# Optimization experiments

Hardware: AMD Instinct MI355X
Metric: run time of the kernel (lower is better)

Reference implementation:

```python
import jax, jax.numpy as jnp
import numpy as np

NUM_GRAPHS = 1024
NODES_PER_GRAPH = 9
EDGES_PER_GRAPH = NODES_PER_GRAPH * (NODES_PER_GRAPH - 1)  # 72, fully connected no self-loops
N = NUM_GRAPHS * NODES_PER_GRAPH
E = NUM_GRAPHS * EDGES_PER_GRAPH
POS_DIM = 64
HID = 256          # gnn_hidden_dim / common_gnn_dim
S1_FEAT = HID      # stage1 feature_dim (after projection)
S1_INT = S1_FEAT + POS_DIM           # 320
S2_FEAT = 2 * HID                    # 512 (two scales concatenated)
S2_OUT = 2 * HID                     # 512
S2_INT = S2_FEAT + POS_DIM           # 576
LN_EPS = 1e-5
SM_EPS = 1e-16  # PyG softmax eps


def _dense(x, w, b):
    return x @ w + b


def _layer_norm(x, g, b):
    mu = jnp.mean(x, axis=-1, keepdims=True)
    var = jnp.mean(jnp.square(x - mu), axis=-1, keepdims=True)
    return (x - mu) * jax.lax.rsqrt(var + LN_EPS) * g + b


def _segment_softmax(logits, idx, n):
    # logits: [E,1]; normalize over edges sharing the same destination node
    m = jax.ops.segment_max(logits, idx, num_segments=n)
    e = jnp.exp(logits - m[idx])
    s = jax.ops.segment_sum(e, idx, num_segments=n)
    return e / (s[idx] + SM_EPS)


def _gnn_layer(x, pos, src, dst, n, p):
    # x: [N, F], pos: [N, P]; edges src->dst (PyG: edge_index[0]=src j, edge_index[1]=dst i)
    ix = jnp.concatenate([x, pos], axis=-1)            # integrated_x [N, F+P]
    ii, ij = ix[dst], ix[src]                          # integrated_x_i / _j per edge
    # pairwise_fn(integrated_x_j, integrated_x_i) -> mlp(cat([integrated_x_i, integrated_x_j]))
    pw_in = jnp.concatenate([ii, ij], axis=-1)         # [E, 2*(F+P)]
    rel = _dense(jax.nn.gelu(_dense(pw_in, p['pw1_w'], p['pw1_b']), approximate=False),
                 p['pw2_w'], p['pw2_b'])               # [E, out]
    att_in = jnp.concatenate([x[dst], x[src], pos[dst], pos[src]], axis=-1)
    logits = _dense(jax.nn.leaky_relu(_dense(att_in, p['att1_w'], p['att1_b']), 0.01),
                    p['att2_w'], p['att2_b'])          # [E, 1]
    attw = _segment_softmax(logits, dst, n)
    aggr = jax.ops.segment_sum(attw * rel, dst, num_segments=n)  # [N, out]
    upd = jax.nn.gelu(_dense(jnp.concatenate([ix, aggr], axis=-1), p['upd_w'], p['upd_b']),
                      approximate=False)
    h = _dense(ix, p['skip_w'], p['skip_b']) + upd
    return _layer_norm(h, p['ln_g'], p['ln_b'])


def _glorot(key, shape):
    fan_in, fan_out = shape[0], shape[1]
    lim = np.sqrt(6.0 / (fan_in + fan_out))
    return jax.random.uniform(key, shape, jnp.float32, -lim, lim)


def setup_inputs() -> dict:
    key = jax.random.key(0)
    ks = iter(jax.random.split(key, 64))

    feat_low = jax.random.normal(next(ks), (N, 512), jnp.float32)
    feat_high = jax.random.normal(next(ks), (N, 1024), jnp.float32)
    batch_indices = jnp.repeat(jnp.arange(NUM_GRAPHS), NODES_PER_GRAPH).astype(jnp.int32)

    # fully connected (no self loop) edges within each 9-node graph
    loc = np.array([(j, i) for i in range(NODES_PER_GRAPH) for j in range(NODES_PER_GRAPH) if i != j],
                   dtype=np.int64)  # (src, dst)
    off = np.repeat(np.arange(NUM_GRAPHS) * NODES_PER_GRAPH, EDGES_PER_GRAPH)
    src = np.tile(loc[:, 0], NUM_GRAPHS) + off
    dst = np.tile(loc[:, 1], NUM_GRAPHS) + off
    edge_index = jnp.asarray(np.stack([src, dst]), dtype=jnp.int32)  # [2, E]

    inp = dict(feat_low=feat_low, feat_high=feat_high,
               batch_indices=batch_indices, edge_index=edge_index)

    inp['pos_table'] = jax.random.normal(next(ks), (NODES_PER_GRAPH, POS_DIM), jnp.float32)
    inp['proj_low_w'] = _glorot(next(ks), (512, HID)); inp['proj_low_b'] = jnp.zeros((HID,), jnp.float32)
    inp['proj_high_w'] = _glorot(next(ks), (1024, HID)); inp['proj_high_b'] = jnp.zeros((HID,), jnp.float32)

    def layer_params(pref, fdim, pdim, out):
        integ = fdim + pdim
        d = {}
        d[pref + 'pw1_w'] = _glorot(next(ks), (2 * integ, out)); d[pref + 'pw1_b'] = jnp.zeros((out,), jnp.float32)
        d[pref + 'pw2_w'] = _glorot(next(ks), (out, out)); d[pref + 'pw2_b'] = jnp.zeros((out,), jnp.float32)
        d[pref + 'att1_w'] = _glorot(next(ks), (2 * fdim + 2 * pdim, out)); d[pref + 'att1_b'] = jnp.zeros((out,), jnp.float32)
        d[pref + 'att2_w'] = _glorot(next(ks), (out, 1)); d[pref + 'att2_b'] = jnp.zeros((1,), jnp.float32)
        d[pref + 'upd_w'] = _glorot(next(ks), (integ + out, out)); d[pref + 'upd_b'] = jnp.zeros((out,), jnp.float32)
        d[pref + 'ln_g'] = jnp.ones((out,), jnp.float32); d[pref + 'ln_b'] = jnp.zeros((out,), jnp.float32)
        d[pref + 'skip_w'] = _glorot(next(ks), (integ, out)); d[pref + 'skip_b'] = jnp.zeros((out,), jnp.float32)
        return d

    inp.update(layer_params('s1_', S1_FEAT, POS_DIM, HID))
    inp.update(layer_params('s2_', S2_FEAT, POS_DIM, S2_OUT))

    inp['cls1_w'] = _glorot(next(ks), (S2_OUT, HID)); inp['cls1_b'] = jnp.zeros((HID,), jnp.float32)
    inp['cls2_w'] = _glorot(next(ks), (HID, 1)); inp['cls2_b'] = jnp.zeros((1,), jnp.float32)
    return inp


def _forward(feat_low, feat_high, pos_table,
             proj_low_w, proj_low_b, proj_high_w, proj_high_b,
             s1, s2, cls1_w, cls1_b, cls2_w, cls2_b,
             batch_indices, edge_index):
    src, dst = edge_index[0], edge_index[1]
    pos_ids = jnp.tile(jnp.arange(NODES_PER_GRAPH), NUM_GRAPHS)
    pos = pos_table[pos_ids]                                  # [N, P]
    h_low = _gnn_layer(_dense(feat_low, proj_low_w, proj_low_b), pos, src, dst, N, s1)
    h_high = _gnn_layer(_dense(feat_high, proj_high_w, proj_high_b), pos, src, dst, N, s1)
    unified = jnp.concatenate([h_low, h_high], axis=-1)       # [N, 512]
    h2 = _gnn_layer(unified, pos, src, dst, N, s2)            # [N, 512]
    pooled = jax.ops.segment_sum(h2, batch_indices, num_segments=NUM_GRAPHS)
    hid = jax.nn.gelu(_dense(pooled, cls1_w, cls1_b), approximate=False)
    return _dense(hid, cls2_w, cls2_b)                        # [G, 1]


S1_KEYS = ['pw1_w', 'pw1_b', 'pw2_w', 'pw2_b', 'att1_w', 'att1_b', 'att2_w', 'att2_b',
           'upd_w', 'upd_b', 'ln_g', 'ln_b', 'skip_w', 'skip_b']


def reference(feat_low, feat_high, batch_indices, edge_index, pos_table,
              proj_low_w, proj_low_b, proj_high_w, proj_high_b,
              s1_pw1_w, s1_pw1_b, s1_pw2_w, s1_pw2_b, s1_att1_w, s1_att1_b,
              s1_att2_w, s1_att2_b, s1_upd_w, s1_upd_b, s1_ln_g, s1_ln_b,
              s1_skip_w, s1_skip_b,
              s2_pw1_w, s2_pw1_b, s2_pw2_w, s2_pw2_b, s2_att1_w, s2_att1_b,
              s2_att2_w, s2_att2_b, s2_upd_w, s2_upd_b, s2_ln_g, s2_ln_b,
              s2_skip_w, s2_skip_b,
              cls1_w, cls1_b, cls2_w, cls2_b):
    s1 = dict(zip(S1_KEYS, [s1_pw1_w, s1_pw1_b, s1_pw2_w, s1_pw2_b, s1_att1_w, s1_att1_b,
                            s1_att2_w, s1_att2_b, s1_upd_w, s1_upd_b, s1_ln_g, s1_ln_b,
                            s1_skip_w, s1_skip_b]))
    s2 = dict(zip(S1_KEYS, [s2_pw1_w, s2_pw1_b, s2_pw2_w, s2_pw2_b, s2_att1_w, s2_att1_b,
                            s2_att2_w, s2_att2_b, s2_upd_w, s2_upd_b, s2_ln_g, s2_ln_b,
                            s2_skip_w, s2_skip_b]))
    return _forward(feat_low, feat_high, pos_table,
                    proj_low_w, proj_low_b, proj_high_w, proj_high_b,
                    s1, s2, cls1_w, cls1_b, cls2_w, cls2_b,
                    batch_indices, edge_index)
```

## Files before the change

### kernel.cpp

```cpp
#include <hip/hip_runtime.h>
#include <math.h>

#define NUM_GRAPHS 1024
#define NPG 9
#define NN 9216
#define NN2 18432
#define POSD 64

typedef __attribute__((ext_vector_type(8))) short bf16x8;
typedef __attribute__((ext_vector_type(4))) float f32x4;

__device__ __forceinline__ float gelu_f(float x) {
    return 0.5f * x * (1.0f + erff(x * 0.70710678118654752f));
}
__device__ __forceinline__ float gelu_fast(float x) {
    float y2 = 1.5957691216f * x * (1.0f + 0.044715f * x * x);
    float t = __expf(fminf(y2, 80.f));
    return x * t * __frcp_rn(t + 1.0f);
}
__device__ __forceinline__ ushort f2b(float v) {
    unsigned u = __float_as_uint(v);
    return (ushort)((u + 0x7fffu + ((u >> 16) & 1u)) >> 16);
}
__device__ __forceinline__ float b2f(ushort u) {
    return __uint_as_float(((unsigned)u) << 16);
}
__device__ __forceinline__ void gload16(const ushort* g, ushort* l) {
    __builtin_amdgcn_global_load_lds((const __attribute__((address_space(1))) void*)g,
                                     (__attribute__((address_space(3))) void*)l, 16, 0, 0);
}

__global__ __launch_bounds__(256, 3) void mgemm(
    const ushort* __restrict__ A, int lda,
    const ushort* __restrict__ Wt, int ldw,
    const float* __restrict__ bias1,
    const float* __restrict__ prow, int ldp,
    ushort* __restrict__ outB, int ldo, int K)
{
    __shared__ ushort smem[24576];
    const int wv = threadIdx.x >> 6, lane = threadIdx.x & 63;
    const int rh = wv & 1, ch = wv >> 1;

    const int GX = gridDim.x;
    const int nwg = GX * gridDim.y;
    const int flat = blockIdx.y * GX + blockIdx.x;
    const int swq = nwg >> 3, swr = nwg & 7;
    const int xcd = flat & 7, posi = flat >> 3;
    const int tix = (xcd < swr ? xcd * (swq + 1) : swr * (swq + 1) + (xcd - swr) * swq) + posi;
    const int m0 = (tix / GX) * 128, n0 = (tix % GX) * 128;

    f32x4 acc[4][4];
#pragma unroll
    for (int i = 0; i < 4; i++)
#pragma unroll
        for (int j = 0; j < 4; j++) acc[i][j] = (f32x4){0.f, 0.f, 0.f, 0.f};

    const ushort* Ab = A + (size_t)m0 * lda;
    const ushort* Wb = Wt + (size_t)n0 * ldw;

    auto stage = [&](int b, int k0) {
        ushort* sA = smem + b * 4096;
        ushort* sB = smem + 12288 + b * 4096;
#pragma unroll
        for (int i = 0; i < 2; i++) {
            int c = wv * 2 + i;
            int u = c * 64 + lane;
            int row = u >> 2, p = u & 3;
            int q = (p - (row >> 1)) & 3;
            gload16(Ab + (size_t)row * lda + k0 + q * 8, sA + c * 512);
            gload16(Wb + (size_t)row * ldw + k0 + q * 8, sB + c * 512);
        }
    };

    const int nsteps = K >> 5;
    stage(0, 0);
    stage(1, 32);
    int cur = 0;
    for (int s = 0; s < nsteps; s++) {
        if (s + 1 < nsteps) {
            asm volatile("s_waitcnt vmcnt(4)" ::: "memory");
        } else {
            asm volatile("s_waitcnt vmcnt(0)" ::: "memory");
        }
        __builtin_amdgcn_s_barrier();
        __builtin_amdgcn_sched_barrier(0);
        if (s + 2 < nsteps) {
            int nb = cur + 2; if (nb >= 3) nb -= 3;
            stage(nb, (s + 2) << 5);
        }

        const ushort* sA = smem + cur * 4096;
        const ushort* sB = smem + 12288 + cur * 4096;
        const int qg = lane >> 4;
        bf16x8 af[4], bfr[4];
#pragma unroll
        for (int bi = 0; bi < 4; bi++) {
            int r = rh * 64 + bi * 16 + (lane & 15);
            af[bi] = *(const bf16x8*)(sA + (r * 4 + ((qg + (r >> 1)) & 3)) * 8);
        }
#pragma unroll
        for (int bj = 0; bj < 4; bj++) {
            int r = ch * 64 + bj * 16 + (lane & 15);
            bfr[bj] = *(const bf16x8*)(sB + (r * 4 + ((qg + (r >> 1)) & 3)) * 8);
        }
        __builtin_amdgcn_s_setprio(1);
#pragma unroll
        for (int bi = 0; bi < 4; bi++)
#pragma unroll
            for (int bj = 0; bj < 4; bj++)
                acc[bi][bj] = __builtin_amdgcn_mfma_f32_16x16x32_bf16(
                    af[bi], bfr[bj], acc[bi][bj], 0, 0, 0);
        __builtin_amdgcn_s_setprio(0);
        __builtin_amdgcn_sched_barrier(0);
        cur++; if (cur >= 3) cur -= 3;
    }

    __syncthreads();
    float* sP = (float*)smem;
    const bool haveP = (prow != 0);
    if (haveP) {
        for (int i = threadIdx.x; i < 9 * 128; i += 256) {
            int rr = i >> 7, c = i & 127;
            sP[rr * 129 + c] = prow[(size_t)rr * ldp + n0 + c] + bias1[n0 + c];
        }
        __syncthreads();
    }
    ushort* T = smem + 4096;
#pragma unroll
    for (int bi = 0; bi < 4; bi++) {
#pragma unroll
        for (int r = 0; r < 4; r++) {
            int row = rh * 64 + bi * 16 + (lane >> 4) * 4 + r;
            int r9 = (m0 + row) % 9;
#pragma unroll
            for (int bj = 0; bj < 4; bj++) {
                int col = ch * 64 + bj * 16 + (lane & 15);
                float v = acc[bi][bj][r];
                if (haveP) v += sP[r9 * 129 + col];
                T[row * 136 + col] = f2b(v);
            }
        }
    }
    __syncthreads();
    {
        int row = threadIdx.x >> 1, half = threadIdx.x & 1;
        const ushort* src = T + row * 136 + half * 64;
        ushort* dst = outB + (size_t)(m0 + row) * ldo + n0 + half * 64;
#pragma unroll
        for (int j = 0; j < 8; j++)
            *(bf16x8*)(dst + j * 8) = *(const bf16x8*)(src + j * 8);
    }
}

struct PJArg {
    const ushort* A[2];
    const ushort* W[2];
    const float*  bias[2];
    ushort*       out[2];
    int lda[2], K[2];
};

__global__ __launch_bounds__(256, 3) void pjgemm(PJArg pa)
{
    __shared__ ushort sA[3][128 * 32];
    __shared__ ushort sB[3][128 * 32];
    const int z = blockIdx.z;
    const ushort* __restrict__ A  = pa.A[z];
    const ushort* __restrict__ Wt = pa.W[z];
    const float*  __restrict__ bias = pa.bias[z];
    ushort* out = pa.out[z];
    const int lda = pa.lda[z], ldw = lda, K = pa.K[z];

    const int wv = threadIdx.x >> 6, lane = threadIdx.x & 63;
    const int rh = wv & 1, ch = wv >> 1;

    const int GX = gridDim.x;
    const int nwg = GX * gridDim.y;
    const int flat = blockIdx.y * GX + blockIdx.x;
    const int swq = nwg >> 3, swr = nwg & 7;
    const int xcd = flat & 7, posi = flat >> 3;
    const int tix = (xcd < swr ? xcd * (swq + 1) : swr * (swq + 1) + (xcd - swr) * swq) + posi;
    const int m0 = (tix / GX) * 128, n0 = (tix % GX) * 128;

    f32x4 acc[4][4];
#pragma unroll
    for (int i = 0; i < 4; i++)
#pragma unroll
        for (int j = 0; j < 4; j++) acc[i][j] = (f32x4){0.f, 0.f, 0.f, 0.f};

    const ushort* Ab = A + (size_t)m0 * lda;
    const ushort* Wb = Wt + (size_t)n0 * ldw;

    auto stage = [&](int b, int k0) {
#pragma unroll
        for (int i = 0; i < 2; i++) {
            int c = wv * 2 + i;
            int u = c * 64 + lane;
            int row = u >> 2, p = u & 3;
            int q = (p - (row >> 1)) & 3;
            gload16(Ab + (size_t)row * lda + k0 + q * 8, sA[b] + c * 512);
            gload16(Wb + (size_t)row * ldw + k0 + q * 8, sB[b] + c * 512);
        }
    };
// ... 45 lines not shown
    __syncthreads();

#pragma unroll
    for (int bi = 0; bi < 4; bi++) {
#pragma unroll
        for (int r = 0; r < 4; r++) {
            int m = m0 + rh * 64 + bi * 16 + (lane >> 4) * 4 + r;
#pragma unroll
            for (int bj = 0; bj < 4; bj++) {
                int nc = ch * 64 + bj * 16 + (lane & 15);
                float v = acc[bi][bj][r] + sBias[nc];
                out[(size_t)m * 512 + n0 + nc] = f2b(v);
            }
        }
    }
}

#define NJOBS 16
struct TJobsArg {
    const float* src[NJOBS];
    long dst[NJOBS];
    int K[NJOBS], N[NJOBS], off0[NJOBS], ldo[NJOBS];
};

__global__ __launch_bounds__(256) void tw_kernel(TJobsArg ja, ushort* wbuf)
{
    int j = blockIdx.y;
    int K = ja.K[j], N = ja.N[j];
    int tk = K >> 5, tn = N >> 5;
    int t = blockIdx.x;
    if (t >= tk * tn) return;
    int kt = t % tk, nt = t / tk;
    const float* src = ja.src[j];
    ushort* out = wbuf + ja.dst[j];
    int ldo = ja.ldo[j];
    __shared__ float L[32][33];
    int r = threadIdx.x >> 5, c = threadIdx.x & 31;
#pragma unroll
    for (int rr = 0; rr < 4; rr++) {
        int k = kt * 32 + rr * 8 + r;
        L[rr * 8 + r][c] = src[(size_t)(ja.off0[j] + k) * N + nt * 32 + c];
    }
    __syncthreads();
#pragma unroll
    for (int rr = 0; rr < 4; rr++) {
        int n = nt * 32 + rr * 8 + r;
        out[(size_t)n * ldo + kt * 32 + c] = f2b(L[c][rr * 8 + r]);
    }
}

template<int O>
__global__ __launch_bounds__(256) void edge_kernel_t(
    const ushort* __restrict__ PB, const float* __restrict__ att2_w,
    ushort* __restrict__ Gout, int ldG, float* __restrict__ S)
{
    constexpr int O2 = O * 2, O5 = O * 5;
    constexpr int tpr = O >> 8;
    constexpr int tcount = 9 * tpr;
    constexpr int nch = O >> 3;
    constexpr int cshift = (O == 256) ? 5 : 6;
    constexpr int E = O >> 6;
    __shared__ ushort sPB[9 * O2];
    __shared__ float sAw[O];
    __shared__ float logits[72];
    __shared__ float aw[72];
    const int g = blockIdx.x;
    const int tid = threadIdx.x, lane = tid & 63, wave = tid >> 6;
    const ushort* gbase = PB + (size_t)g * 9 * O5;

    for (int i = wave; i < tcount; i += 4) {
        int row = i / tpr, co = i - row * tpr;
        gload16(gbase + (size_t)row * O5 + O2 + co * 512 + lane * 8, sPB + i * 512);
    }
    for (int c = tid; c < O; c += 256) sAw[c] = att2_w[c];
    __syncthreads();

    for (int e = wave; e < 72; e += 4) {
        int d = e >> 3, k = e & 7;
        int s = k + (k >= d);
        const ushort* ad = sPB + d * O2 + lane * E;
        const ushort* as = sPB + s * O2 + O + lane * E;
        const float* wp = sAw + lane * E;
        float p = 0.f;
        if constexpr (E == 4) {
            ushort4 a4 = *(const ushort4*)ad;
            ushort4 s4 = *(const ushort4*)as;
            float4 w4 = *(const float4*)wp;
            const ushort* ap = (const ushort*)&a4;
            const ushort* sp = (const ushort*)&s4;
            const float* wf = (const float*)&w4;
#pragma unroll
            for (int j = 0; j < 4; j++) {
                float v = b2f(ap[j]) + b2f(sp[j]);
                v = fmaxf(v, 0.01f * v);
                p += v * wf[j];
            }
        } else {
            bf16x8 a8 = *(const bf16x8*)ad;
            bf16x8 s8 = *(const bf16x8*)as;
            float4 w0 = *(const float4*)wp;
            float4 w1 = *(const float4*)(wp + 4);
            const ushort* ap = (const ushort*)&a8;
            const ushort* sp = (const ushort*)&s8;
            const float wf[8] = {w0.x, w0.y, w0.z, w0.w, w1.x, w1.y, w1.z, w1.w};
#pragma unroll
            for (int j = 0; j < 8; j++) {
                float v = b2f(ap[j]) + b2f(sp[j]);
                v = fmaxf(v, 0.01f * v);
                p += v * wf[j];
            }
        }
#pragma unroll
        for (int off = 32; off; off >>= 1) p += __shfl_down(p, off, 64);
        if (lane == 0) logits[e] = p;
    }
    __syncthreads();

    for (int i = wave; i < tcount; i += 4) {
        int row = i / tpr, co = i - row * tpr;
        gload16(gbase + (size_t)row * O5 + co * 512 + lane * 8, sPB + i * 512);
    }

    if (tid < 9) {
        float m = -INFINITY;
#pragma unroll
        for (int k = 0; k < 8; k++) m = fmaxf(m, logits[tid * 8 + k]);
        float s = 0.f, ee[8];
#pragma unroll
        for (int k = 0; k < 8; k++) { ee[k] = expf(logits[tid * 8 + k] - m); s += ee[k]; }
        float inv = 1.0f / (s + 1e-16f);
#pragma unroll
        for (int k = 0; k < 8; k++) aw[tid * 8 + k] = ee[k] * inv;
        S[g * 9 + tid] = s * inv;
    }
    __syncthreads();

    for (int idx = tid; idx < 9 * nch; idx += 256) {
        int n = idx >> cshift, cc = idx & (nch - 1);
        bf16x8 pdv = *(const bf16x8*)(sPB + n * O2 + cc * 8);
        const ushort* pp = (const ushort*)&pdv;
        float pdf[8];
#pragma unroll
        for (int j = 0; j < 8; j++) pdf[j] = b2f(pp[j]);
        float acc8[8];
#pragma unroll
        for (int j = 0; j < 8; j++) acc8[j] = 0.f;
#pragma unroll
        for (int k = 0; k < 8; k++) {
            int s = k + (k >= n);
            float w = aw[n * 8 + k];
            bf16x8 psv = *(const bf16x8*)(sPB + s * O2 + O + cc * 8);
            const ushort* qp = (const ushort*)&psv;
#pragma unroll
            for (int j = 0; j < 8; j++)
                acc8[j] += w * gelu_fast(pdf[j] + b2f(qp[j]));
        }
        ushort o8[8];
#pragma unroll
        for (int j = 0; j < 8; j++) o8[j] = f2b(acc8[j]);
        *(bf16x8*)(Gout + (size_t)(g * 9 + n) * ldG + cc * 8) = *(const bf16x8*)o8;
    }
}

__global__ __launch_bounds__(256) void ln_kernel(
    const ushort* __restrict__ P0,
    const float* __restrict__ ub, const float* __restrict__ vb,
    const float* __restrict__ S, const float* __restrict__ posU,
    const ushort* __restrict__ PBs, int ld5,
    const float* __restrict__ gw, const float* __restrict__ bw,
    ushort* outB, int ldoB, int rowsplit, float* outF, int O)
{
    const int wid = threadIdx.x >> 6, lane = threadIdx.x & 63;
    const int n = blockIdx.x * 4 + wid;
    const float sv = S[n];
    const ushort* p0 = P0 + (size_t)n * O;
    const ushort* sr = PBs + (size_t)n * ld5;
    const float* pu = posU + (size_t)(n % 9) * O;
    const int q = O >> 6;
    const int c0 = lane * q;

    float vals[8];
    float sum = 0.f;
    if (O == 256) {
        ushort4 pv = *(const ushort4*)(p0 + c0);
        ushort4 sk = *(const ushort4*)(sr + c0);
        float4 uu = *(const float4*)(ub + c0);
        float4 vv = *(const float4*)(vb + c0);
        float4 gg = *(const float4*)(pu + c0);
        const ushort tp[4] = {pv.x, pv.y, pv.z, pv.w};
        const ushort ts[4] = {sk.x, sk.y, sk.z, sk.w};
        const float tu[4] = {uu.x, uu.y, uu.z, uu.w};
        const float tv[4] = {vv.x, vv.y, vv.z, vv.w};
        const float tg[4] = {gg.x, gg.y, gg.z, gg.w};
#pragma unroll
        for (int j = 0; j < 4; j++) {
            float t = b2f(tp[j]) + tu[j] + tv[j] * sv + tg[j];
            vals[j] = gelu_f(t) + b2f(ts[j]);
            sum += vals[j];
        }
    } else {
        bf16x8 pv = *(const bf16x8*)(p0 + c0);
        bf16x8 sk = *(const bf16x8*)(sr + c0);
        const ushort* tp = (const ushort*)&pv;
        const ushort* ts = (const ushort*)&sk;
        float4 u0 = *(const float4*)(ub + c0), u1 = *(const float4*)(ub + c0 + 4);
        float4 v0 = *(const float4*)(vb + c0), v1 = *(const float4*)(vb + c0 + 4);
        float4 g0 = *(const float4*)(pu + c0), g1 = *(const float4*)(pu + c0 + 4);
        const float tu[8] = {u0.x,u0.y,u0.z,u0.w, u1.x,u1.y,u1.z,u1.w};
        const float tv[8] = {v0.x,v0.y,v0.z,v0.w, v1.x,v1.y,v1.z,v1.w};
        const float tg[8] = {g0.x,g0.y,g0.z,g0.w, g1.x,g1.y,g1.z,g1.w};
#pragma unroll
        for (int j = 0; j < 8; j++) {
            float t = b2f(tp[j]) + tu[j] + tv[j] * sv + tg[j];
            vals[j] = gelu_f(t) + b2f(ts[j]);
            sum += vals[j];
        }
    }

#pragma unroll
    for (int off = 32; off; off >>= 1) sum += __shfl_xor(sum, off, 64);
    const float mu = sum / (float)O;
    float var = 0.f;
#pragma unroll
    for (int j = 0; j < 8; j++) {
        if (j < q) { float d = vals[j] - mu; var += d * d; }
    }
#pragma unroll
    for (int off = 32; off; off >>= 1) var += __shfl_xor(var, off, 64);
    const float rstd = rsqrtf(var / (float)O + 1e-5f);

    int orow = n, coloff = 0;
    if (n >= rowsplit) { orow = n - rowsplit; coloff = 256; }

    if (outB) {
        ushort o[8];
#pragma unroll
        for (int j = 0; j < 8; j++) {
            if (j < q) o[j] = f2b((vals[j] - mu) * rstd * gw[c0 + j] + bw[c0 + j]);
        }
        ushort* dst = outB + (size_t)orow * ldoB + coloff + c0;
        if (q == 4) *(ushort4*)dst = *(const ushort4*)o;
        else        *(bf16x8*)dst = *(const bf16x8*)o;
    }
    if (outF) {
        float* dst = outF + (size_t)n * O + c0;
#pragma unroll
        for (int j = 0; j < 8; j++) {
            if (j < q) dst[j] = (vals[j] - mu) * rstd * gw[c0 + j] + bw[c0 + j];
        }
    }
}

__global__ void prep_kernel(
    const float* __restrict__ pw1_b1, const float* __restrict__ att1_b1, const float* __restrict__ skip_b1,
    const float* __restrict__ pw1_b2, const float* __restrict__ att1_b2, const float* __restrict__ skip_b2,
    const float* __restrict__ pos_table,
    const float* __restrict__ s1_pw1, const float* __restrict__ s1_att, const float* __restrict__ s1_skp,
    const float* __restrict__ s2_pw1, const float* __restrict__ s2_att, const float* __restrict__ s2_skp,
    const float* __restrict__ pw2_b1, const float* __restrict__ upd_w1,
    const float* __restrict__ pw2_b2, const float* __restrict__ upd_w2,
    const float* __restrict__ pw2_w1, const float* __restrict__ pw2_w2,
    const float* __restrict__ feat_low, const float* __restrict__ feat_high,
    float* biasC1, float* biasC2,
    float* posPB1, float* posPB2, float* posU1, float* posU2,
    float* vb1, float* vb2, ushort* pw2f1, ushort* pw2f2, ushort* featB)
{
// ... 97 lines not shown
        ushort4 o;
        o.x = f2b(v.x); o.y = f2b(v.y); o.z = f2b(v.z); o.w = f2b(v.w);
        ((ushort4*)(featB + (size_t)NN * 512))[i] = o;
    }
}

__global__ __launch_bounds__(256) void head_kernel(
    const float* __restrict__ h2,
    const float* __restrict__ cls1_w, const float* __restrict__ cls1_b,
    const float* __restrict__ cls2_w, const float* __restrict__ cls2_b,
    float* __restrict__ out)
{
    __shared__ float pooled[4][512];
    __shared__ float hid[4][256];
    const int b = blockIdx.x, tid = threadIdx.x;

    for (int idx = tid; idx < 4 * 512; idx += 256) {
        int gi = idx >> 9, c = idx & 511;
        const float* base = h2 + (size_t)((b * 4 + gi) * 9) * 512 + c;
        float s = 0.f;
#pragma unroll
        for (int k = 0; k < NPG; k++) s += base[(size_t)k * 512];
        pooled[gi][c] = s;
    }
    __syncthreads();

    {
        float acc[4] = {0.f, 0.f, 0.f, 0.f};
        for (int c = 0; c < 512; c++) {
            float w = cls1_w[(size_t)c * 256 + tid];
#pragma unroll
            for (int gi = 0; gi < 4; gi++) acc[gi] += pooled[gi][c] * w;
        }
        float bb = cls1_b[tid];
#pragma unroll
        for (int gi = 0; gi < 4; gi++) hid[gi][tid] = gelu_f(acc[gi] + bb);
    }
    __syncthreads();

    {
        int gi = tid >> 6, lane = tid & 63;
        float p = 0.f;
#pragma unroll
        for (int i = 0; i < 4; i++) p += hid[gi][lane + 64 * i] * cls2_w[lane + 64 * i];
#pragma unroll
        for (int off = 32; off; off >>= 1) p += __shfl_down(p, off, 64);
        if (lane == 0) out[b * 4 + gi] = p + cls2_b[0];
    }
}

static inline void mg(hipStream_t st, int M, int N, int K,
                      const ushort* A, int lda, const ushort* Wt, int ldw,
                      const float* bias1, const float* prow, int ldp,
                      ushort* outB, int ldo)
{
    dim3 grid(N / 128, M / 128);
    mgemm<<<grid, dim3(256), 0, st>>>(A, lda, Wt, ldw, bias1, prow, ldp,
                                      outB, ldo, K);
}

extern "C" void kernel_launch(void* const* d_in, const int* in_sizes, int n_in,
                              void* d_out, int out_size, void* d_ws, size_t ws_size,
                              hipStream_t stream)
{
    (void)in_sizes; (void)n_in; (void)out_size; (void)ws_size;
    const float* feat_low   = (const float*)d_in[0];
    const float* feat_high  = (const float*)d_in[1];
    const float* pos_table  = (const float*)d_in[4];
    const float* proj_low_w  = (const float*)d_in[5];
    const float* proj_low_b  = (const float*)d_in[6];
    const float* proj_high_w = (const float*)d_in[7];
    const float* proj_high_b = (const float*)d_in[8];
    const float* cls1_w = (const float*)d_in[37];
    const float* cls1_b = (const float*)d_in[38];
    const float* cls2_w = (const float*)d_in[39];
    const float* cls2_b = (const float*)d_in[40];
    float* out = (float*)d_out;

    const float* s1_pw1 = (const float*)d_in[9];
    const float* s1_att = (const float*)d_in[13];
    const float* s1_upd = (const float*)d_in[17];
    const float* s1_skp = (const float*)d_in[21];
    const float* s2_pw1 = (const float*)d_in[23];
    const float* s2_att = (const float*)d_in[27];
    const float* s2_upd = (const float*)d_in[31];
    const float* s2_skp = (const float*)d_in[35];

    const float* att2_w1 = (const float*)d_in[15];
    const float* upd_b1  = (const float*)d_in[18];
    const float* ln_g1   = (const float*)d_in[19];
    const float* ln_b1   = (const float*)d_in[20];
    const float* att2_w2 = (const float*)d_in[29];
    const float* upd_b2  = (const float*)d_in[32];
    const float* ln_g2   = (const float*)d_in[33];
    const float* ln_b2   = (const float*)d_in[34];

    char* base = (char*)d_ws;
    size_t cur = 0;
    auto alloc = [&](size_t bytes) { void* p = base + cur; cur += (bytes + 255) & ~(size_t)255; return p; };
    void*   PBreg = alloc((size_t)NN * 2560 * 2);
    ushort* PB    = (ushort*)PBreg;
    ushort* featB = (ushort*)PBreg;
    void*   IX1reg = alloc((size_t)NN2 * 512 * 2);
    ushort* ixa1  = (ushort*)IX1reg;
    float*  h2    = (float*)IX1reg;
    ushort* ixa2  = (ushort*)alloc((size_t)NN * 1024 * 2);
    ushort* PT    = (ushort*)alloc((size_t)NN2 * 512 * 2);
    float*  S     = (float*)alloc((size_t)NN2 * 4);
    float*  biasC1 = (float*)alloc(1280 * 4);
    float*  biasC2 = (float*)alloc(2560 * 4);
    float*  posPB1 = (float*)alloc(9 * 1280 * 4);
    float*  posPB2 = (float*)alloc(9 * 2560 * 4);
    float*  posU1  = (float*)alloc(9 * 256 * 4);
    float*  posU2  = (float*)alloc(9 * 512 * 4);
    float*  vb1   = (float*)alloc(256 * 4);
    float*  vb2   = (float*)alloc(512 * 4);
    ushort* wbuf  = (ushort*)alloc((size_t)3400000 * 2);

    TJobsArg ja;
    long woff[16];
    {
        struct J { const float* s; int K, N, off0, ldo; long sz; };
        J js[NJOBS] = {
            {proj_low_w,  512, 256, 0, 512, 512L * 256},
            {proj_high_w, 1024, 256, 0, 1024, 1024L * 256},
            {s1_pw1, 256, 256, 0, 256, 256L * 256},
            {s1_pw1, 256, 256, 320, 256, 256L * 256},
            {s1_att, 256, 256, 0, 256, 256L * 256},
            {s1_att, 256, 256, 256, 256, 256L * 256},
            {s1_skp, 256, 256, 0, 256, 256L * 256},
            {s1_upd, 256, 256, 0, 512, 512L * 256},
            {s1_upd, 256, 256, 320, 256, 256L * 256},
            {s2_pw1, 512, 512, 0, 512, 512L * 512},
            {s2_pw1, 512, 512, 576, 512, 512L * 512},
            {s2_att, 512, 512, 0, 512, 512L * 512},
            {s2_att, 512, 512, 512, 512, 512L * 512},
            {s2_skp, 512, 512, 0, 512, 512L * 512},
            {s2_upd, 512, 512, 0, 1024, 1024L * 512},
            {s2_upd, 512, 512, 576, 512, 512L * 512},
        };
        long off = 0;
        for (int i = 0; i < NJOBS; i++) {
            ja.src[i] = js[i].s; ja.K[i] = js[i].K; ja.N[i] = js[i].N;
            ja.off0[i] = js[i].off0; ja.ldo[i] = js[i].ldo;
            ja.dst[i] = off; woff[i] = off;
            off += js[i].sz;
        }
    }
    long pw2off1 = woff[15] + 512L * 512;
    long pw2off2 = pw2off1 + 256L * 256;
    tw_kernel<<<dim3(256, NJOBS), dim3(256), 0, stream>>>(ja, wbuf);

    ushort* wBig5_1 = wbuf + woff[2];
    ushort* updW1   = wbuf + woff[7];
    ushort* updbT1  = wbuf + woff[8];
    ushort* wBig5_2 = wbuf + woff[9];
    ushort* updW2   = wbuf + woff[14];
    ushort* updbT2  = wbuf + woff[15];
    ushort* pw2f1   = wbuf + pw2off1;
    ushort* pw2f2   = wbuf + pw2off2;

    {
        long tot = 1280 + 2560 + 9 * 1280 + 9 * 2560 + 9 * 256 + 9 * 512
                 + 256 + 512 + 256 * 256 + 512 * 512
                 + (long)NN * 512 / 4 + (long)NN * 1024 / 4;
        prep_kernel<<<dim3((unsigned)((tot + 255) / 256)), dim3(256), 0, stream>>>(
            (const float*)d_in[10], (const float*)d_in[14], (const float*)d_in[22],
            (const float*)d_in[24], (const float*)d_in[28], (const float*)d_in[36],
            pos_table,
            s1_pw1, s1_att, s1_skp, s2_pw1, s2_att, s2_skp,
            (const float*)d_in[12], s1_upd, (const float*)d_in[26], s2_upd,
            (const float*)d_in[11], (const float*)d_in[25],
            feat_low, feat_high,
            biasC1, biasC2, posPB1, posPB2, posU1, posU2, vb1, vb2, pw2f1, pw2f2, featB);
    }

    mg(stream, 256, 256, 256, updbT1, 256, pw2f1, 256, 0, 0, 0, updW1 + 256, 512);
    mg(stream, 512, 512, 512, updbT2, 512, pw2f2, 512, 0, 0, 0, updW2 + 512, 1024);

    {
        PJArg pa;
        pa.A[0] = featB;                      pa.lda[0] = 512;  pa.K[0] = 512;
        pa.A[1] = featB + (size_t)NN * 512;   pa.lda[1] = 1024; pa.K[1] = 1024;
        pa.W[0] = wbuf + woff[0];
        pa.W[1] = wbuf + woff[1];
        pa.bias[0] = proj_low_b;
        pa.bias[1] = proj_high_b;
        pa.out[0] = ixa1;
        pa.out[1] = ixa1 + (size_t)NN * 512;
        pjgemm<<<dim3(2, NN / 128, 2), dim3(256), 0, stream>>>(pa);
    }

    mg(stream, NN2, 1280, 256, ixa1, 512, wBig5_1, 256, biasC1, posPB1, 1280, PB, 1280);
    edge_kernel_t<256><<<dim3(2 * NUM_GRAPHS), dim3(256), 0, stream>>>(
        PB, att2_w1, ixa1 + 256, 512, S);
    mg(stream, NN2, 256, 512, ixa1, 512, updW1, 512, 0, 0, 0, PT, 256);
    ln_kernel<<<dim3(NN2 / 4), dim3(256), 0, stream>>>(
        PT, upd_b1, vb1, S, posU1,
        PB + 4 * 256, 1280, ln_g1, ln_b1, ixa2, 1024, NN, 0, 256);

    mg(stream, NN, 2560, 512, ixa2, 1024, wBig5_2, 512, biasC2, posPB2, 2560, PB, 2560);
    edge_kernel_t<512><<<dim3(NUM_GRAPHS), dim3(256), 0, stream>>>(
        PB, att2_w2, ixa2 + 512, 1024, S);
    mg(stream, NN, 512, 1024, ixa2, 1024, updW2, 1024, 0, 0, 0, PT, 512);
    ln_kernel<<<dim3(NN / 4), dim3(256), 0, stream>>>(
        PT, upd_b2, vb2, S, posU2,
        PB + 4 * 512, 2560, ln_g2, ln_b2, 0, 0, 1 << 30, h2, 512);

    head_kernel<<<dim3(NUM_GRAPHS / 4), dim3(256), 0, stream>>>(h2, cls1_w, cls1_b, cls2_w, cls2_b, out);
}
```

Baseline: 522.6 us.

## Enlarge mgemm tile to 256x128 with 8 waves and double buffering

The general GEMM kernel now uses 512 threads (8 waves) per block, each block covering 256 rows by 128 columns, so each staged weight tile is reused across twice as many rows. The three-stage LDS pipeline becomes a two-buffer scheme that waits on all outstanding loads every step. The epilogue writes the output in two 128-row passes through shared memory. This cuts weight reloads and halves the number of blocks, at the cost of less latency hiding in the K loop and fewer blocks, which can leave CUs idle when M is small.

```diff
diff --git a/kernel.cpp b/kernel.cpp
--- a/kernel.cpp
+++ b/kernel.cpp
@@ -30,7 +30,7 @@
                                      (__attribute__((address_space(3))) void*)l, 16, 0, 0);
 }
 
-__global__ __launch_bounds__(256, 3) void mgemm(
+__global__ __launch_bounds__(512, 4) void mgemm(
     const ushort* __restrict__ A, int lda,
     const ushort* __restrict__ Wt, int ldw,
     const float* __restrict__ bias1,
@@ -39,7 +39,7 @@
 {
     __shared__ ushort smem[24576];
     const int wv = threadIdx.x >> 6, lane = threadIdx.x & 63;
-    const int rh = wv & 1, ch = wv >> 1;
+    const int wr = wv >> 1, wc = wv & 1;
 
     const int GX = gridDim.x;
     const int nwg = GX * gridDim.y;
@@ -47,7 +47,7 @@
     const int swq = nwg >> 3, swr = nwg & 7;
     const int xcd = flat & 7, posi = flat >> 3;
     const int tix = (xcd < swr ? xcd * (swq + 1) : swr * (swq + 1) + (xcd - swr) * swq) + posi;
-    const int m0 = (tix / GX) * 128, n0 = (tix % GX) * 128;
+    const int m0 = (tix / GX) * 256, n0 = (tix % GX) * 128;
 
     f32x4 acc[4][4];
 #pragma unroll
@@ -59,8 +59,8 @@
     const ushort* Wb = Wt + (size_t)n0 * ldw;
 
     auto stage = [&](int b, int k0) {
-        ushort* sA = smem + b * 4096;
-        ushort* sB = smem + 12288 + b * 4096;
+        ushort* sA = smem + b * 8192;
+        ushort* sB = smem + 16384 + b * 4096;
 #pragma unroll
         for (int i = 0; i < 2; i++) {
             int c = wv * 2 + i;
@@ -68,39 +68,36 @@
             int row = u >> 2, p = u & 3;
             int q = (p - (row >> 1)) & 3;
             gload16(Ab + (size_t)row * lda + k0 + q * 8, sA + c * 512);
+        }
+        {
+            int c = wv;
+            int u = c * 64 + lane;
+            int row = u >> 2, p = u & 3;
+            int q = (p - (row >> 1)) & 3;
             gload16(Wb + (size_t)row * ldw + k0 + q * 8, sB + c * 512);
         }
     };
 
     const int nsteps = K >> 5;
     stage(0, 0);
-    stage(1, 32);
-    int cur = 0;
     for (int s = 0; s < nsteps; s++) {
-        if (s + 1 < nsteps) {
-            asm volatile("s_waitcnt vmcnt(4)" ::: "memory");
-        } else {
-            asm volatile("s_waitcnt vmcnt(0)" ::: "memory");
-        }
+        asm volatile("s_waitcnt vmcnt(0)" ::: "memory");
         __builtin_amdgcn_s_barrier();
         __builtin_amdgcn_sched_barrier(0);
-        if (s + 2 < nsteps) {
-            int nb = cur + 2; if (nb >= 3) nb -= 3;
-            stage(nb, (s + 2) << 5);
-        }
-
-        const ushort* sA = smem + cur * 4096;
-        const ushort* sB = smem + 12288 + cur * 4096;
+        if (s + 1 < nsteps) stage((s + 1) & 1, (s + 1) << 5);
+
+        const ushort* sA = smem + (s & 1) * 8192;
+        const ushort* sB = smem + 16384 + (s & 1) * 4096;
         const int qg = lane >> 4;
         bf16x8 af[4], bfr[4];
 #pragma unroll
         for (int bi = 0; bi < 4; bi++) {
-            int r = rh * 64 + bi * 16 + (lane & 15);
+            int r = wr * 64 + bi * 16 + (lane & 15);
             af[bi] = *(const bf16x8*)(sA + (r * 4 + ((qg + (r >> 1)) & 3)) * 8);
         }
 #pragma unroll
         for (int bj = 0; bj < 4; bj++) {
-            int r = ch * 64 + bj * 16 + (lane & 15);
+            int r = wc * 64 + bj * 16 + (lane & 15);
             bfr[bj] = *(const bf16x8*)(sB + (r * 4 + ((qg + (r >> 1)) & 3)) * 8);
         }
         __builtin_amdgcn_s_setprio(1);
@@ -112,43 +109,50 @@
                     af[bi], bfr[bj], acc[bi][bj], 0, 0, 0);
         __builtin_amdgcn_s_setprio(0);
         __builtin_amdgcn_sched_barrier(0);
-        cur++; if (cur >= 3) cur -= 3;
     }
 
     __syncthreads();
     float* sP = (float*)smem;
     const bool haveP = (prow != 0);
     if (haveP) {
-        for (int i = threadIdx.x; i < 9 * 128; i += 256) {
+        for (int i = threadIdx.x; i < 9 * 128; i += 512) {
             int rr = i >> 7, c = i & 127;
             sP[rr * 129 + c] = prow[(size_t)rr * ldp + n0 + c] + bias1[n0 + c];
         }
         __syncthreads();
     }
-    ushort* T = smem + 4096;
-#pragma unroll
-    for (int bi = 0; bi < 4; bi++) {
-#pragma unroll
-        for (int r = 0; r < 4; r++) {
-            int row = rh * 64 + bi * 16 + (lane >> 4) * 4 + r;
-            int r9 = (m0 + row) % 9;
-#pragma unroll
-            for (int bj = 0; bj < 4; bj++) {
-                int col = ch * 64 + bj * 16 + (lane & 15);
-                float v = acc[bi][bj][r];
-                if (haveP) v += sP[r9 * 129 + col];
-                T[row * 136 + col] = f2b(v);
+    ushort* T = smem + 2560;
+#pragma unroll
+    for (int pass = 0; pass < 2; pass++) {
+        if ((wv >> 2) == pass) {
+            int rbase = (wr & 1) * 64;
+#pragma unroll
+            for (int bi = 0; bi < 4; bi++) {
+#pragma unroll
+                for (int r = 0; r < 4; r++) {
+                    int row_l = rbase + bi * 16 + (lane >> 4) * 4 + r;
+                    int r9 = (m0 + pass * 128 + row_l) % 9;
+#pragma unroll
+                    for (int bj = 0; bj < 4; bj++) {
+                        int col = wc * 64 + bj * 16 + (lane & 15);
+                        float v = acc[bi][bj][r];
+                        if (haveP) v += sP[r9 * 129 + col];
+                        T[row_l * 136 + col] = f2b(v);
+                    }
+                }
             }
         }
-    }
-    __syncthreads();
-    {
-        int row = threadIdx.x >> 1, half = threadIdx.x & 1;
-        const ushort* src = T + row * 136 + half * 64;
-        ushort* dst = outB + (size_t)(m0 + row) * ldo + n0 + half * 64;
-#pragma unroll
-        for (int j = 0; j < 8; j++)
-            *(bf16x8*)(dst + j * 8) = *(const bf16x8*)(src + j * 8);
+        __syncthreads();
+        {
+            int row_l = threadIdx.x >> 2, qq = threadIdx.x & 3;
+            const ushort* src = T + row_l * 136 + qq * 32;
+            ushort* dst = outB + (size_t)(m0 + pass * 128 + row_l) * ldo + n0 + qq * 32;
+            *(bf16x8*)(dst) = *(const bf16x8*)(src);
+            *(bf16x8*)(dst + 8) = *(const bf16x8*)(src + 8);
+            *(bf16x8*)(dst + 16) = *(const bf16x8*)(src + 16);
+            *(bf16x8*)(dst + 24) = *(const bf16x8*)(src + 24);
+        }
+        if (pass == 0) __syncthreads();
     }
 }
 
@@ -665,8 +669,8 @@
                       const float* bias1, const float* prow, int ldp,
                       ushort* outB, int ldo)
 {
-    dim3 grid(N / 128, M / 128);
-    mgemm<<<grid, dim3(256), 0, st>>>(A, lda, Wt, ldw, bias1, prow, ldp,
+    dim3 grid(N / 128, M / 256);
+    mgemm<<<grid, dim3(512), 0, st>>>(A, lda, Wt, ldw, bias1, prow, ldp,
                                       outB, ldo, K);
 }
 
```

Result: slower. 537.6 us (+2.9%).

## Make mgemm waves independent 64x64 tiles with per-wave double-buffered LDS

Applied to the files above, without the earlier changes.

The GEMM kernel moves from one 128x128 tile per block, with four waves sharing a triple-buffered LDS pipeline, to each wave owning its own 64x64 output tile with a private double-buffered LDS region. This removes all block-level barriers in the main loop and the epilogue, and the launch becomes a flattened 1D grid with XCD swizzle over wave tiles. The cost is that operand tiles are no longer shared across waves, so global and LDS traffic per FLOP roughly doubles. Occupancy hints also drop from 3 to 2 blocks per CU.

```diff
diff --git a/kernel.cpp b/kernel.cpp
--- a/kernel.cpp
+++ b/kernel.cpp
@@ -30,24 +30,25 @@
                                      (__attribute__((address_space(3))) void*)l, 16, 0, 0);
 }
 
-__global__ __launch_bounds__(256, 3) void mgemm(
+__global__ __launch_bounds__(256, 2) void mgemm(
     const ushort* __restrict__ A, int lda,
     const ushort* __restrict__ Wt, int ldw,
     const float* __restrict__ bias1,
     const float* __restrict__ prow, int ldp,
-    ushort* __restrict__ outB, int ldo, int K)
+    ushort* __restrict__ outB, int ldo, int K, int NT)
 {
-    __shared__ ushort smem[24576];
+    __shared__ ushort smem[4][8192];
     const int wv = threadIdx.x >> 6, lane = threadIdx.x & 63;
-    const int rh = wv & 1, ch = wv >> 1;
-
-    const int GX = gridDim.x;
-    const int nwg = GX * gridDim.y;
-    const int flat = blockIdx.y * GX + blockIdx.x;
+    ushort* wb = smem[wv];
+
+    const int nwg = gridDim.x;
+    const int flat = blockIdx.x;
     const int swq = nwg >> 3, swr = nwg & 7;
     const int xcd = flat & 7, posi = flat >> 3;
-    const int tix = (xcd < swr ? xcd * (swq + 1) : swr * (swq + 1) + (xcd - swr) * swq) + posi;
-    const int m0 = (tix / GX) * 128, n0 = (tix % GX) * 128;
+    const int btix = (xcd < swr ? xcd * (swq + 1) : swr * (swq + 1) + (xcd - swr) * swq) + posi;
+    const int w = btix * 4 + wv;
+    const int mt = w / NT, nt = w - mt * NT;
+    const int m0 = mt * 64, n0 = nt * 64;
 
     f32x4 acc[4][4];
 #pragma unroll
@@ -59,48 +60,41 @@
     const ushort* Wb = Wt + (size_t)n0 * ldw;
 
     auto stage = [&](int b, int k0) {
-        ushort* sA = smem + b * 4096;
-        ushort* sB = smem + 12288 + b * 4096;
-#pragma unroll
-        for (int i = 0; i < 2; i++) {
-            int c = wv * 2 + i;
-            int u = c * 64 + lane;
-            int row = u >> 2, p = u & 3;
+#pragma unroll
+        for (int c = 0; c < 4; c++) {
+            int row = c * 16 + (lane >> 2), p = lane & 3;
             int q = (p - (row >> 1)) & 3;
-            gload16(Ab + (size_t)row * lda + k0 + q * 8, sA + c * 512);
-            gload16(Wb + (size_t)row * ldw + k0 + q * 8, sB + c * 512);
+            gload16(Ab + (size_t)row * lda + k0 + q * 8, wb + b * 2048 + c * 512);
+        }
+#pragma unroll
+        for (int c = 0; c < 4; c++) {
+            int row = c * 16 + (lane >> 2), p = lane & 3;
+            int q = (p - (row >> 1)) & 3;
+            gload16(Wb + (size_t)row * ldw + k0 + q * 8, wb + 4096 + b * 2048 + c * 512);
         }
     };
 
     const int nsteps = K >> 5;
     stage(0, 0);
-    stage(1, 32);
-    int cur = 0;
     for (int s = 0; s < nsteps; s++) {
         if (s + 1 < nsteps) {
-            asm volatile("s_waitcnt vmcnt(4)" ::: "memory");
+            stage((s + 1) & 1, (s + 1) << 5);
+            asm volatile("s_waitcnt vmcnt(8)" ::: "memory");
         } else {
             asm volatile("s_waitcnt vmcnt(0)" ::: "memory");
         }
-        __builtin_amdgcn_s_barrier();
-        __builtin_amdgcn_sched_barrier(0);
-        if (s + 2 < nsteps) {
-            int nb = cur + 2; if (nb >= 3) nb -= 3;
-            stage(nb, (s + 2) << 5);
-        }
-
-        const ushort* sA = smem + cur * 4096;
-        const ushort* sB = smem + 12288 + cur * 4096;
+        const ushort* sA = wb + (s & 1) * 2048;
+        const ushort* sB = wb + 4096 + (s & 1) * 2048;
         const int qg = lane >> 4;
         bf16x8 af[4], bfr[4];
 #pragma unroll
         for (int bi = 0; bi < 4; bi++) {
-            int r = rh * 64 + bi * 16 + (lane & 15);
+            int r = bi * 16 + (lane & 15);
             af[bi] = *(const bf16x8*)(sA + (r * 4 + ((qg + (r >> 1)) & 3)) * 8);
         }
 #pragma unroll
         for (int bj = 0; bj < 4; bj++) {
-            int r = ch * 64 + bj * 16 + (lane & 15);
+            int r = bj * 16 + (lane & 15);
             bfr[bj] = *(const bf16x8*)(sB + (r * 4 + ((qg + (r >> 1)) & 3)) * 8);
         }
         __builtin_amdgcn_s_setprio(1);
@@ -111,44 +105,38 @@
                 acc[bi][bj] = __builtin_amdgcn_mfma_f32_16x16x32_bf16(
                     af[bi], bfr[bj], acc[bi][bj], 0, 0, 0);
         __builtin_amdgcn_s_setprio(0);
-        __builtin_amdgcn_sched_barrier(0);
-        cur++; if (cur >= 3) cur -= 3;
-    }
-
-    __syncthreads();
-    float* sP = (float*)smem;
+    }
+
+    float* sP = (float*)wb;
     const bool haveP = (prow != 0);
     if (haveP) {
-        for (int i = threadIdx.x; i < 9 * 128; i += 256) {
-            int rr = i >> 7, c = i & 127;
-            sP[rr * 129 + c] = prow[(size_t)rr * ldp + n0 + c] + bias1[n0 + c];
-        }
-        __syncthreads();
-    }
-    ushort* T = smem + 4096;
+#pragma unroll
+        for (int i = 0; i < 9; i++)
+            sP[i * 64 + lane] = prow[(size_t)i * ldp + n0 + lane] + bias1[n0 + lane];
+    }
+    ushort* T = wb + 1280;
 #pragma unroll
     for (int bi = 0; bi < 4; bi++) {
 #pragma unroll
         for (int r = 0; r < 4; r++) {
-            int row = rh * 64 + bi * 16 + (lane >> 4) * 4 + r;
+            int row = bi * 16 + (lane >> 4) * 4 + r;
             int r9 = (m0 + row) % 9;
 #pragma unroll
             for (int bj = 0; bj < 4; bj++) {
-                int col = ch * 64 + bj * 16 + (lane & 15);
+                int col = bj * 16 + (lane & 15);
                 float v = acc[bi][bj][r];
-                if (haveP) v += sP[r9 * 129 + col];
-                T[row * 136 + col] = f2b(v);
+                if (haveP) v += sP[r9 * 64 + col];
+                T[row * 68 + col] = f2b(v);
             }
         }
     }
-    __syncthreads();
-    {
-        int row = threadIdx.x >> 1, half = threadIdx.x & 1;
-        const ushort* src = T + row * 136 + half * 64;
-        ushort* dst = outB + (size_t)(m0 + row) * ldo + n0 + half * 64;
-#pragma unroll
-        for (int j = 0; j < 8; j++)
-            *(bf16x8*)(dst + j * 8) = *(const bf16x8*)(src + j * 8);
+#pragma unroll
+    for (int p4 = 0; p4 < 4; p4++) {
+        int row = p4 * 16 + (lane >> 2), cq = (lane & 3) * 16;
+        const ushort* src = T + row * 68 + cq;
+        ushort* dst = outB + (size_t)(m0 + row) * ldo + n0 + cq;
+        *(bf16x8*)dst = *(const bf16x8*)src;
+        *(bf16x8*)(dst + 8) = *(const bf16x8*)(src + 8);
     }
 }
 
@@ -665,9 +653,10 @@
                       const float* bias1, const float* prow, int ldp,
                       ushort* outB, int ldo)
 {
-    dim3 grid(N / 128, M / 128);
-    mgemm<<<grid, dim3(256), 0, st>>>(A, lda, Wt, ldw, bias1, prow, ldp,
-                                      outB, ldo, K);
+    int NT = N / 64;
+    int nblk = (M / 64) * NT / 4;
+    mgemm<<<dim3(nblk), dim3(256), 0, st>>>(A, lda, Wt, ldw, bias1, prow, ldp,
+                                            outB, ldo, K, NT);
 }
 
 extern "C" void kernel_launch(void* const* d_in, const int* in_sizes, int n_in,
```

Measured after the change: 535.3 us. 2.4% more time.

## Fuse update GEMM into big projection GEMM and edge kernel

Applied to the files above, without the earlier changes.

The x-part of the update linear layer now runs as extra N-tiles of the large per-node projection GEMM, selected by a split column index that switches the weight and output pointers. The aggregated-message part of the update GEMM runs inside the edge kernel as a small MFMA product on the per-graph aggregation held in LDS, so the aggregation no longer goes out to global memory. The layer-norm kernel sums both partial products. This removes one separate GEMM launch per stage and a round trip of the aggregation buffer. In exchange, the edge kernel reads weights straight from global memory for each graph, does extra MFMA work padded to 16 rows for 9 nodes, and uses more LDS.

```diff
diff --git a/kernel.cpp b/kernel.cpp
--- a/kernel.cpp
+++ b/kernel.cpp
@@ -35,7 +35,9 @@
     const ushort* __restrict__ Wt, int ldw,
     const float* __restrict__ bias1,
     const float* __restrict__ prow, int ldp,
-    ushort* __restrict__ outB, int ldo, int K)
+    ushort* __restrict__ outB, int ldo, int K,
+    int splitN, const ushort* __restrict__ Wt2, int ldw2,
+    ushort* __restrict__ outB2, int ldo2)
 {
     __shared__ ushort smem[24576];
     const int wv = threadIdx.x >> 6, lane = threadIdx.x & 63;
@@ -49,6 +51,13 @@
     const int tix = (xcd < swr ? xcd * (swq + 1) : swr * (swq + 1) + (xcd - swr) * swq) + posi;
     const int m0 = (tix / GX) * 128, n0 = (tix % GX) * 128;
 
+    const bool isSplit = (n0 >= splitN);
+    const ushort* WtS = isSplit ? Wt2 : Wt;
+    const int ldwS    = isSplit ? ldw2 : ldw;
+    ushort* outS      = isSplit ? outB2 : outB;
+    const int ldoS    = isSplit ? ldo2 : ldo;
+    const int nc0     = isSplit ? (n0 - splitN) : n0;
+
     f32x4 acc[4][4];
 #pragma unroll
     for (int i = 0; i < 4; i++)
@@ -56,7 +65,7 @@
         for (int j = 0; j < 4; j++) acc[i][j] = (f32x4){0.f, 0.f, 0.f, 0.f};
 
     const ushort* Ab = A + (size_t)m0 * lda;
-    const ushort* Wb = Wt + (size_t)n0 * ldw;
+    const ushort* Wb = WtS + (size_t)nc0 * ldwS;
 
     auto stage = [&](int b, int k0) {
         ushort* sA = smem + b * 4096;
@@ -68,7 +77,7 @@
             int row = u >> 2, p = u & 3;
             int q = (p - (row >> 1)) & 3;
             gload16(Ab + (size_t)row * lda + k0 + q * 8, sA + c * 512);
-            gload16(Wb + (size_t)row * ldw + k0 + q * 8, sB + c * 512);
+            gload16(Wb + (size_t)row * ldwS + k0 + q * 8, sB + c * 512);
         }
     };
 
@@ -117,7 +126,7 @@
 
     __syncthreads();
     float* sP = (float*)smem;
-    const bool haveP = (prow != 0);
+    const bool haveP = (prow != 0) && !isSplit;
     if (haveP) {
         for (int i = threadIdx.x; i < 9 * 128; i += 256) {
             int rr = i >> 7, c = i & 127;
@@ -145,7 +154,7 @@
     {
         int row = threadIdx.x >> 1, half = threadIdx.x & 1;
         const ushort* src = T + row * 136 + half * 64;
-        ushort* dst = outB + (size_t)(m0 + row) * ldo + n0 + half * 64;
+        ushort* dst = outS + (size_t)(m0 + row) * ldoS + nc0 + half * 64;
 #pragma unroll
         for (int j = 0; j < 8; j++)
             *(bf16x8*)(dst + j * 8) = *(const bf16x8*)(src + j * 8);
@@ -300,7 +309,8 @@
 template<int O>
 __global__ __launch_bounds__(256) void edge_kernel_t(
     const ushort* __restrict__ PB, const float* __restrict__ att2_w,
-    ushort* __restrict__ Gout, int ldG, float* __restrict__ S)
+    const ushort* __restrict__ Wg, int ldwg,
+    ushort* __restrict__ Pg, int ldpg, float* __restrict__ S)
 {
     constexpr int O2 = O * 2, O5 = O * 5;
     constexpr int tpr = O >> 8;
@@ -308,13 +318,18 @@
     constexpr int nch = O >> 3;
     constexpr int cshift = (O == 256) ? 5 : 6;
     constexpr int E = O >> 6;
+    constexpr int GLD = O + 8;
+    constexpr int NTW = (O / 16) / 4;
     __shared__ ushort sPB[9 * O2];
+    __shared__ ushort Gl[16 * GLD];
     __shared__ float sAw[O];
     __shared__ float logits[72];
     __shared__ float aw[72];
     const int g = blockIdx.x;
     const int tid = threadIdx.x, lane = tid & 63, wave = tid >> 6;
     const ushort* gbase = PB + (size_t)g * 9 * O5;
+
+    for (int i = tid; i < 7 * GLD; i += 256) Gl[9 * GLD + i] = 0;
 
     for (int i = wave; i < tcount; i += 4) {
         int row = i / tpr, co = i - row * tpr;
@@ -406,12 +421,37 @@
         ushort o8[8];
 #pragma unroll
         for (int j = 0; j < 8; j++) o8[j] = f2b(acc8[j]);
-        *(bf16x8*)(Gout + (size_t)(g * 9 + n) * ldG + cc * 8) = *(const bf16x8*)o8;
+        *(bf16x8*)(Gl + n * GLD + cc * 8) = *(const bf16x8*)o8;
+    }
+    __syncthreads();
+
+    {
+        const int l15 = lane & 15, qg = lane >> 4;
+        const ushort* aRow = Gl + l15 * GLD + qg * 8;
+#pragma unroll
+        for (int i = 0; i < NTW; i++) {
+            int nt16 = (wave * NTW + i) * 16;
+            const ushort* bRow = Wg + (size_t)(nt16 + l15) * ldwg + qg * 8;
+            f32x4 gacc = (f32x4){0.f, 0.f, 0.f, 0.f};
+#pragma unroll
+            for (int kk = 0; kk < O / 32; kk++) {
+                bf16x8 afr = *(const bf16x8*)(aRow + kk * 32);
+                bf16x8 bfr = *(const bf16x8*)(bRow + kk * 32);
+                gacc = __builtin_amdgcn_mfma_f32_16x16x32_bf16(afr, bfr, gacc, 0, 0, 0);
+            }
+            int rbase = qg * 4;
+#pragma unroll
+            for (int r = 0; r < 4; r++) {
+                int node = rbase + r;
+                if (node < 9)
+                    Pg[(size_t)(g * 9 + node) * ldpg + nt16 + l15] = f2b(gacc[r]);
+            }
+        }
     }
 }
 
 __global__ __launch_bounds__(256) void ln_kernel(
-    const ushort* __restrict__ P0,
+    const ushort* __restrict__ P0, const ushort* __restrict__ P1,
     const float* __restrict__ ub, const float* __restrict__ vb,
     const float* __restrict__ S, const float* __restrict__ posU,
     const ushort* __restrict__ PBs, int ld5,
@@ -422,6 +462,7 @@
     const int n = blockIdx.x * 4 + wid;
     const float sv = S[n];
     const ushort* p0 = P0 + (size_t)n * O;
+    const ushort* p1 = P1 + (size_t)n * O;
     const ushort* sr = PBs + (size_t)n * ld5;
     const float* pu = posU + (size_t)(n % 9) * O;
     const int q = O >> 6;
@@ -431,25 +472,29 @@
     float sum = 0.f;
     if (O == 256) {
         ushort4 pv = *(const ushort4*)(p0 + c0);
+        ushort4 qv = *(const ushort4*)(p1 + c0);
         ushort4 sk = *(const ushort4*)(sr + c0);
         float4 uu = *(const float4*)(ub + c0);
         float4 vv = *(const float4*)(vb + c0);
         float4 gg = *(const float4*)(pu + c0);
         const ushort tp[4] = {pv.x, pv.y, pv.z, pv.w};
+        const ushort tq[4] = {qv.x, qv.y, qv.z, qv.w};
         const ushort ts[4] = {sk.x, sk.y, sk.z, sk.w};
         const float tu[4] = {uu.x, uu.y, uu.z, uu.w};
         const float tv[4] = {vv.x, vv.y, vv.z, vv.w};
         const float tg[4] = {gg.x, gg.y, gg.z, gg.w};
 #pragma unroll
         for (int j = 0; j < 4; j++) {
-            float t = b2f(tp[j]) + tu[j] + tv[j] * sv + tg[j];
+            float t = b2f(tp[j]) + b2f(tq[j]) + tu[j] + tv[j] * sv + tg[j];
             vals[j] = gelu_f(t) + b2f(ts[j]);
             sum += vals[j];
         }
     } else {
         bf16x8 pv = *(const bf16x8*)(p0 + c0);
+        bf16x8 qv = *(const bf16x8*)(p1 + c0);
         bf16x8 sk = *(const bf16x8*)(sr + c0);
         const ushort* tp = (const ushort*)&pv;
+        const ushort* tq = (const ushort*)&qv;
         const ushort* ts = (const ushort*)&sk;
         float4 u0 = *(const float4*)(ub + c0), u1 = *(const float4*)(ub + c0 + 4);
         float4 v0 = *(const float4*)(vb + c0), v1 = *(const float4*)(vb + c0 + 4);
@@ -459,7 +504,7 @@
         const float tg[8] = {g0.x,g0.y,g0.z,g0.w, g1.x,g1.y,g1.z,g1.w};
 #pragma unroll
         for (int j = 0; j < 8; j++) {
-            float t = b2f(tp[j]) + tu[j] + tv[j] * sv + tg[j];
+            float t = b2f(tp[j]) + b2f(tq[j]) + tu[j] + tv[j] * sv + tg[j];
             vals[j] = gelu_f(t) + b2f(ts[j]);
             sum += vals[j];
         }
@@ -663,11 +708,13 @@
 static inline void mg(hipStream_t st, int M, int N, int K,
                       const ushort* A, int lda, const ushort* Wt, int ldw,
                       const float* bias1, const float* prow, int ldp,
-                      ushort* outB, int ldo)
+                      ushort* outB, int ldo,
+                      int splitN = (1 << 30), const ushort* Wt2 = 0, int ldw2 = 0,
+                      ushort* outB2 = 0, int ldo2 = 0)
 {
     dim3 grid(N / 128, M / 128);
     mgemm<<<grid, dim3(256), 0, st>>>(A, lda, Wt, ldw, bias1, prow, ldp,
-                                      outB, ldo, K);
+                                      outB, ldo, K, splitN, Wt2, ldw2, outB2, ldo2);
 }
 
 extern "C" void kernel_launch(void* const* d_in, const int* in_sizes, int n_in,
@@ -727,6 +774,11 @@
     float*  vb1   = (float*)alloc(256 * 4);
     float*  vb2   = (float*)alloc(512 * 4);
     ushort* wbuf  = (ushort*)alloc((size_t)3400000 * 2);
+
+    ushort* PTx1 = PT;
+    ushort* PTg1 = PT + (size_t)NN2 * 256;
+    ushort* PTx2 = PT;
+    ushort* PTg2 = PT + (size_t)NN * 512;
 
     TJobsArg ja;
     long woff[16];
@@ -802,20 +854,20 @@
         pjgemm<<<dim3(2, NN / 128, 2), dim3(256), 0, stream>>>(pa);
     }
 
-    mg(stream, NN2, 1280, 256, ixa1, 512, wBig5_1, 256, biasC1, posPB1, 1280, PB, 1280);
+    mg(stream, NN2, 1536, 256, ixa1, 512, wBig5_1, 256, biasC1, posPB1, 1280,
+       PB, 1280, 1280, updW1, 512, PTx1, 256);
     edge_kernel_t<256><<<dim3(2 * NUM_GRAPHS), dim3(256), 0, stream>>>(
-        PB, att2_w1, ixa1 + 256, 512, S);
-    mg(stream, NN2, 256, 512, ixa1, 512, updW1, 512, 0, 0, 0, PT, 256);
+        PB, att2_w1, updW1 + 256, 512, PTg1, 256, S);
     ln_kernel<<<dim3(NN2 / 4), dim3(256), 0, stream>>>(
-        PT, upd_b1, vb1, S, posU1,
+        PTx1, PTg1, upd_b1, vb1, S, posU1,
         PB + 4 * 256, 1280, ln_g1, ln_b1, ixa2, 1024, NN, 0, 256);
 
-    mg(stream, NN, 2560, 512, ixa2, 1024, wBig5_2, 512, biasC2, posPB2, 2560, PB, 2560);
+    mg(stream, NN, 3072, 512, ixa2, 1024, wBig5_2, 512, biasC2, posPB2, 2560,
+       PB, 2560, 2560, updW2, 1024, PTx2, 512);
     edge_kernel_t<512><<<dim3(NUM_GRAPHS), dim3(256), 0, stream>>>(
-        PB, att2_w2, ixa2 + 512, 1024, S);
-    mg(stream, NN, 512, 1024, ixa2, 1024, updW2, 1024, 0, 0, 0, PT, 512);
+        PB, att2_w2, updW2 + 512, 1024, PTg2, 512, S);
     ln_kernel<<<dim3(NN / 4), dim3(256), 0, stream>>>(
-        PT, upd_b2, vb2, S, posU2,
+        PTx2, PTg2, upd_b2, vb2, S, posU2,
         PB + 4 * 512, 2560, ln_g2, ln_b2, 0, 0, 1 << 30, h2, 512);
 
     head_kernel<<<dim3(NUM_GRAPHS / 4), dim3(256), 0, stream>>>(h2, cls1_w, cls1_b, cls2_w, cls2_b, out);
```

Result: slower. 558.8 us (+6.9%).
